# Kernel optimization log

Measured on AMD Instinct MI355X. Metric: run time of the kernel, lower is better.

## Reference

```python
import jax, jax.numpy as jnp
import numpy as np

EMB = 2048
HD = 64            # head_dim
NH = 32            # n_heads
NKV = 8            # n_kv_groups
GS = NH // NKV     # group_size = 4
WIN = 128          # sliding_window
LAYER_IDX = 0      # even -> sliding-window mask active
ROPE_BASE = 10000.0
MAX_SEQ = 4096
YARN_ORIG = 1024.0
YARN_SCALE = 4.0
YARN_BETA_FAST = 32.0
YARN_BETA_SLOW = 1.0


def _rope_tables():
    # YaRN-adjusted RoPE tables, shape [MAX_SEQ, HD]
    freqs = 1.0 / ROPE_BASE ** (np.arange(0, HD, 2, dtype=np.float32) / HD)
    wave_len = 2.0 * np.pi / freqs
    low = YARN_ORIG / YARN_BETA_FAST
    high = YARN_ORIG / YARN_BETA_SLOW
    t = np.clip((wave_len - low) / (high - low), 0.0, 1.0)
    eff = freqs * (1.0 - t) + (freqs / YARN_SCALE) * t
    conc = 0.1 * np.log(YARN_SCALE) + 1.0
    ang = (np.arange(MAX_SEQ, dtype=np.float32)[:, None] * eff[None, :]) * conc
    ang = np.concatenate([ang, ang], axis=-1).astype(np.float32)
    return jnp.sin(ang), jnp.cos(ang)


def _apply_rope(x, sin, cos):
    # x: [B, H, S, D]; sin/cos: [B, S, D] -> broadcast over heads
    sin = sin[:, None, :, :]
    cos = cos[:, None, :, :]
    x1 = x[..., : HD // 2]
    x2 = x[..., HD // 2 :]
    rotated = jnp.concatenate([-x2, x1], axis=-1)
    return x * cos + rotated * sin


def setup_inputs() -> dict:
    key = jax.random.key(0)
    ks = jax.random.split(key, 8)
    B, S = 2, 2048
    s = 0.02
    x = jax.random.normal(ks[0], (B, S, EMB), dtype=jnp.float32)
    Wq = jax.random.normal(ks[1], (NH * HD, EMB), dtype=jnp.float32) * s
    Wk = jax.random.normal(ks[2], (NKV * HD, EMB), dtype=jnp.float32) * s
    Wv = jax.random.normal(ks[3], (NKV * HD, EMB), dtype=jnp.float32) * s
    Wo = jax.random.normal(ks[4], (EMB, NH * HD), dtype=jnp.float32) * s
    bq = jnp.zeros((NH * HD,), dtype=jnp.float32)
    bk = jnp.zeros((NKV * HD,), dtype=jnp.float32)
    bv = jnp.zeros((NKV * HD,), dtype=jnp.float32)
    bo = jnp.zeros((EMB,), dtype=jnp.float32)
    sinks = jax.random.normal(ks[5], (1, NH, 1, 1), dtype=jnp.float32)
    position_ids = jnp.arange(B * S, dtype=jnp.int64 if jax.config.jax_enable_x64 else jnp.int32).reshape(B, S)
    return {"x": x, "Wq": Wq, "bq": bq, "Wk": Wk, "bk": bk, "Wv": Wv, "bv": bv,
            "Wo": Wo, "bo": bo, "sinks": sinks, "position_ids": position_ids}


def reference(x, Wq, bq, Wk, bk, Wv, bv, Wo, bo, sinks, position_ids):
    B, S, _ = x.shape
    sin_t, cos_t = _rope_tables()
    sin = sin_t[position_ids]  # [B, S, HD]
    cos = cos_t[position_ids]

    Q = (x @ Wq.T + bq).reshape(B, S, NH, HD).transpose(0, 2, 1, 3)    # [B,NH,S,D]
    K = (x @ Wk.T + bk).reshape(B, S, NKV, HD).transpose(0, 2, 1, 3)   # [B,NKV,S,D]
    V = (x @ Wv.T + bv).reshape(B, S, NKV, HD).transpose(0, 2, 1, 3)

    Q = _apply_rope(Q, sin, cos)
    K = _apply_rope(K, sin, cos)

    # GQA without materializing repeated K/V: group query heads by kv group
    Qg = Q.reshape(B, NKV, GS, S, HD)
    scores = jnp.einsum('bgqsd,bgtd->bgqst', Qg, K) / np.sqrt(HD).astype(np.float32)

    i = jnp.arange(S)[:, None]
    j = jnp.arange(S)[None, :]
    allowed = (j <= i) & (j > i - WIN)
    scores = jnp.where(allowed, scores, -jnp.inf)

    # attention-sink logit prepended before softmax, then dropped
    sink = jnp.broadcast_to(sinks.reshape(1, NKV, GS, 1, 1), (B, NKV, GS, S, 1))
    full = jnp.concatenate([sink, scores], axis=-1)
    attn = jax.nn.softmax(full, axis=-1)[..., 1:]

    ctx = jnp.einsum('bgqst,bgtd->bgqsd', attn, V)
    ctx = ctx.reshape(B, NH, S, HD).transpose(0, 2, 1, 3).reshape(B, S, NH * HD)
    out = ctx @ Wo.T + bo
    return out
```

## Files before the change

### kernel.cpp

```cpp
#include <hip/hip_runtime.h>

typedef unsigned short u16;
typedef __bf16 bf16x8 __attribute__((ext_vector_type(8)));
typedef float f32x4 __attribute__((ext_vector_type(4)));
typedef unsigned short us8 __attribute__((ext_vector_type(8)));

__device__ inline u16 f2bf(float f) {
    union { float f; unsigned u; } v; v.f = f;
    unsigned r = v.u + 0x7FFFu + ((v.u >> 16) & 1u);
    return (u16)(r >> 16);
}
__device__ inline float bf2f(u16 h) {
    union { unsigned u; float f; } v; v.u = ((unsigned)h) << 16;
    return v.f;
}
__device__ inline f32x4 mfma16(bf16x8 a, bf16x8 b, f32x4 c) {
    return __builtin_amdgcn_mfma_f32_16x16x32_bf16(a, b, c, 0, 0, 0);
}
__device__ inline void gload_lds16(const u16* g, u16* l) {
    __builtin_amdgcn_global_load_lds(
        (const __attribute__((address_space(1))) void*)g,
        (__attribute__((address_space(3))) void*)l, 16, 0, 0);
}

__global__ __launch_bounds__(256)
void pack_bf16(const float* __restrict__ src, u16* __restrict__ dst, int n)
{
    int i = (blockIdx.x * 256 + threadIdx.x) * 4;
    if (i >= n) return;
    float4 v = *(const float4*)(src + i);
    ushort4 w;
    w.x = f2bf(v.x); w.y = f2bf(v.y); w.z = f2bf(v.z); w.w = f2bf(v.w);
    *(ushort4*)(dst + i) = w;
}

__global__ __launch_bounds__(256)
void concat_bias(const float* __restrict__ bq, const float* __restrict__ bk,
                 const float* __restrict__ bv, float* __restrict__ dst)
{
    int i = blockIdx.x * 256 + threadIdx.x;
    float v;
    if (i < 2048) v = bq[i];
    else if (i < 2560) v = bk[i - 2048];
    else v = bv[i - 2560];
    dst[i] = v;
}

template<int OUT_BF16>
__global__ __launch_bounds__(256, 2)
void gemm_bb(const u16* __restrict__ A, const u16* __restrict__ B,
             const float* __restrict__ bias, void* __restrict__ Yv,
             int M, int N, int K)
{
    __shared__ u16 As[128 * 32];
    __shared__ u16 Bs[128 * 32];
    const int tid = threadIdx.x;
    const int lane = tid & 63;
    const int wv = tid >> 6;
    const int wr = wv >> 1, wc = wv & 1;
    const long m0 = (long)blockIdx.y * 128;
    const long n0 = (long)blockIdx.x * 128;
    const int cc = lane & 15, qq = lane >> 4;

    const int srow = (2 * wv) * 16 + (lane >> 2);
    const int gcol = (((lane & 3) ^ ((lane >> 3) & 3)) << 3);
    const u16* Ag0 = A + (m0 + srow) * (long)K + gcol;
    const u16* Ag1 = A + (m0 + srow + 16) * (long)K + gcol;
    const u16* Bg0 = B + (n0 + srow) * (long)K + gcol;
    const u16* Bg1 = B + (n0 + srow + 16) * (long)K + gcol;
    u16* AsW0 = &As[(2 * wv) * 512];
    u16* AsW1 = AsW0 + 512;
    u16* BsW0 = &Bs[(2 * wv) * 512];
    u16* BsW1 = BsW0 + 512;

    const int csw = (qq ^ ((cc >> 1) & 3)) << 3;

    f32x4 acc[4][4];
#pragma unroll
    for (int i = 0; i < 4; i++)
#pragma unroll
        for (int j = 0; j < 4; j++) acc[i][j] = (f32x4){0.f, 0.f, 0.f, 0.f};

    for (int k0 = 0; k0 < K; k0 += 32) {
        gload_lds16(Ag0 + k0, AsW0);
        gload_lds16(Ag1 + k0, AsW1);
        gload_lds16(Bg0 + k0, BsW0);
        gload_lds16(Bg1 + k0, BsW1);
        __syncthreads();
        bf16x8 af[4], bfr[4];
#pragma unroll
        for (int i = 0; i < 4; i++)
            af[i] = *(const bf16x8*)&As[(wr * 64 + i * 16 + cc) * 32 + csw];
#pragma unroll
        for (int j = 0; j < 4; j++)
            bfr[j] = *(const bf16x8*)&Bs[(wc * 64 + j * 16 + cc) * 32 + csw];
#pragma unroll
        for (int i = 0; i < 4; i++)
#pragma unroll
            for (int j = 0; j < 4; j++)
                acc[i][j] = mfma16(af[i], bfr[j], acc[i][j]);
        __syncthreads();
    }

#pragma unroll
    for (int i = 0; i < 4; i++) {
#pragma unroll
        for (int j = 0; j < 4; j++) {
            long row = m0 + wr * 64 + i * 16 + qq * 4;
            long col = n0 + wc * 64 + j * 16 + cc;
            float bv = bias[col];
#pragma unroll
            for (int r2 = 0; r2 < 4; r2++) {
                float v = acc[i][j][r2] + bv;
                if (OUT_BF16)
                    ((u16*)Yv)[(row + r2) * (long)N + col] = f2bf(v);
                else
                    ((float*)Yv)[(row + r2) * (long)N + col] = v;
            }
        }
    }
}

__global__ __launch_bounds__(256)
void rope_qk(const u16* __restrict__ Yt, const int* __restrict__ pid,
             u16* __restrict__ Out, int nh, int lg, int coff)
{
    int idx = blockIdx.x * 256 + threadIdx.x;
    int d = idx & 31;
    int t2 = idx >> 5;
    int hh = t2 & (nh - 1);
    int m = t2 >> lg;
    const u16* row = Yt + (size_t)m * 3072 + coff + (hh << 6);
    float x1 = bf2f(row[d]), x2 = bf2f(row[d + 32]);
    int pos = pid[m];
    float ex = (float)d * (1.0f / 32.0f);
    float freq = powf(10000.0f, -ex);
    float wl = 6.2831853071795864f / freq;
    float tt = (wl - 32.0f) * (1.0f / 992.0f);
    tt = fminf(fmaxf(tt, 0.0f), 1.0f);
    float eff = freq * (1.0f - tt) + 0.25f * freq * tt;
    float ang = ((float)pos * eff) * 1.1386294361119891f;
    float sv = sinf(ang), cv = cosf(ang);
    int b = m >> 11, s = m & 2047;
    u16* o = Out + (((size_t)(b * nh + hh)) * 2048 + s) * 64;
    o[d]      = f2bf(x1 * cv - x2 * sv);
    o[d + 32] = f2bf(x2 * cv + x1 * sv);
}

__global__ __launch_bounds__(256)
void v_transpose(const u16* __restrict__ Vt, u16* __restrict__ VbT)
{
    __shared__ u16 tile[64][66];
    int s0 = blockIdx.x * 64;
    int bkv = blockIdx.y;
    int b = bkv >> 3, kv = bkv & 7;
    int t = threadIdx.x;
#pragma unroll
    for (int it = 0; it < 16; ++it) {
        int idx = t + it * 256;
        int s = idx >> 6, d = idx & 63;
        tile[s][d] = Vt[((size_t)(b * 2048 + s0 + s)) * 3072 + 2560 + kv * 64 + d];
    }
    __syncthreads();
#pragma unroll
    for (int it = 0; it < 16; ++it) {
        int idx = t + it * 256;
        int d = idx >> 6, s = idx & 63;
        VbT[((size_t)(bkv * 64 + d)) * 2048 + s0 + s] = tile[s][d];
    }
}

__global__ __launch_bounds__(256, 2)
void attn_win(const u16* __restrict__ Qb, const u16* __restrict__ Kb,
              const u16* __restrict__ VbT, const float* __restrict__ sinks,
              u16* __restrict__ Ctx)
{
    __shared__ u16 Ks[192 * 72];
    __shared__ u16 Vs[64 * 200];
    __shared__ u16 Pb[4 * 16 * 200];
    const int S = 2048;
    const int tid = threadIdx.x;
    const int lane = tid & 63;
    const int w = tid >> 6;
    const int cc = lane & 15, qq = lane >> 4;
    const int blk = blockIdx.x;
    const int qt = blk & 31;
    const int bkv = blk >> 5;
    const int b = bkv >> 3, kv = bkv & 7;
    const int q0 = qt * 64;
    const int ks0 = q0 - 128;
    const int h = kv * 4 + w;

    const u16* KbBase = Kb + (size_t)bkv * S * 64;
#pragma unroll
    for (int it = 0; it < 6; ++it) {
        int c = tid + it * 256;
        int kk = c >> 3, c8 = (c & 7) << 3;
        int sk = ks0 + kk;
        us8 v = {0, 0, 0, 0, 0, 0, 0, 0};
        if (sk >= 0) v = *(const us8*)(KbBase + (size_t)sk * 64 + c8);
        *(us8*)&Ks[kk * 72 + c8] = v;
    }
    const u16* VtBase = VbT + (size_t)bkv * 64 * S;
#pragma unroll
    for (int it = 0; it < 6; ++it) {
        int c = tid + it * 256;
        int d = c / 24, kc = c % 24;
        int kk0 = kc << 3;
        int sk = ks0 + kk0;
        us8 v = {0, 0, 0, 0, 0, 0, 0, 0};
        if (sk >= 0) v = *(const us8*)(VtBase + (size_t)d * S + sk);
        *(us8*)&Vs[d * 200 + kk0] = v;
    }
    __syncthreads();

    const float sinkv = sinks[h];
    u16* Pw = &Pb[w * 3200];
    const u16* Qbase = Qb + ((size_t)(b * 32 + h) * S + q0) * 64;

    for (int i = 0; i < 4; ++i) {
        const u16* Qrow = Qbase + (size_t)(i * 16 + cc) * 64;
        bf16x8 aq0 = *(const bf16x8*)(Qrow + qq * 8);
        bf16x8 aq1 = *(const bf16x8*)(Qrow + 32 + qq * 8);

        f32x4 sc[12];
#pragma unroll
        for (int j = 0; j < 12; j++) sc[j] = (f32x4){0.f, 0.f, 0.f, 0.f};
#pragma unroll
        for (int j = 0; j < 12; j++) {
            bf16x8 b0 = *(const bf16x8*)&Ks[(j * 16 + cc) * 72 + qq * 8];
            bf16x8 b1 = *(const bf16x8*)&Ks[(j * 16 + cc) * 72 + 32 + qq * 8];
            sc[j] = mfma16(aq0, b0, sc[j]);
            sc[j] = mfma16(aq1, b1, sc[j]);
        }

#pragma unroll
        for (int r = 0; r < 4; ++r) {
            int qi = i * 16 + qq * 4 + r;
            float sval[12];
            float mx = -3.0e38f;
#pragma unroll
            for (int j = 0; j < 12; j++) {
                int kk = j * 16 + cc;
                float s = sc[j][r] * 0.125f;
                bool ok = (kk > qi) && (kk <= qi + 128) && (ks0 + kk >= 0);
                s = ok ? s : -3.0e38f;
                sval[j] = s;
                mx = fmaxf(mx, s);
            }
#pragma unroll
            for (int off = 1; off < 16; off <<= 1) mx = fmaxf(mx, __shfl_xor(mx, off));
            mx = fmaxf(mx, sinkv);
            float sum = 0.f;
#pragma unroll
            for (int j = 0; j < 12; j++) {
                float p = __expf(sval[j] - mx);
                sval[j] = p;
                sum += p;
            }
#pragma unroll
            for (int off = 1; off < 16; off <<= 1) sum += __shfl_xor(sum, off);
            float rden = 1.0f / (sum + __expf(sinkv - mx));
#pragma unroll
            for (int j = 0; j < 12; j++)
                Pw[(qq * 4 + r) * 200 + j * 16 + cc] = f2bf(sval[j] * rden);
        }

        f32x4 o[4];
#pragma unroll
        for (int jt = 0; jt < 4; jt++) o[jt] = (f32x4){0.f, 0.f, 0.f, 0.f};
#pragma unroll
        for (int ks = 0; ks < 6; ks++) {
            bf16x8 ap = *(const bf16x8*)&Pw[cc * 200 + ks * 32 + qq * 8];
#pragma unroll
            for (int jt = 0; jt < 4; jt++) {
                bf16x8 bv = *(const bf16x8*)&Vs[(jt * 16 + cc) * 200 + ks * 32 + qq * 8];
                o[jt] = mfma16(ap, bv, o[jt]);
            }
        }
#pragma unroll
        for (int jt = 0; jt < 4; jt++) {
#pragma unroll
            for (int r = 0; r < 4; r++) {
                size_t off = ((size_t)(b * S + q0 + i * 16 + qq * 4 + r)) * 2048
                           + h * 64 + jt * 16 + cc;
                Ctx[off] = f2bf(o[jt][r]);
            }
        }
    }
}

extern "C" void kernel_launch(void* const* d_in, const int* in_sizes, int n_in,
                              void* d_out, int out_size, void* d_ws, size_t ws_size,
                              hipStream_t stream)
{
    const float* x    = (const float*)d_in[0];
    const float* Wq   = (const float*)d_in[1];
    const float* bq   = (const float*)d_in[2];
    const float* Wk   = (const float*)d_in[3];
    const float* bk   = (const float*)d_in[4];
    const float* Wv   = (const float*)d_in[5];
    const float* bv   = (const float*)d_in[6];
    const float* Wo   = (const float*)d_in[7];
    const float* bo   = (const float*)d_in[8];
    const float* sinks = (const float*)d_in[9];
    const int*   pid  = (const int*)d_in[10];
    float* out = (float*)d_out;

    char* ws = (char*)d_ws;
    u16*   Wqkvb = (u16*)ws;
    u16*   Wob   = (u16*)(ws + 12582912);
    u16*   xQb   = (u16*)(ws + 20971520);
    u16*   QKV   = (u16*)(ws + 37748736);
    u16*   Kb    = (u16*)(ws + 62914560);
    u16*   VbT   = (u16*)(ws + 67108864);
    float* bqkv  = (float*)(ws + 71303168);

    const int M = 4096;
    pack_bf16<<<8192, 256, 0, stream>>>(x,  xQb, 8388608);
    pack_bf16<<<4096, 256, 0, stream>>>(Wq, Wqkvb, 4194304);
    pack_bf16<<<1024, 256, 0, stream>>>(Wk, Wqkvb + 4194304, 1048576);
    pack_bf16<<<1024, 256, 0, stream>>>(Wv, Wqkvb + 5242880, 1048576);
    pack_bf16<<<4096, 256, 0, stream>>>(Wo, Wob, 4194304);
    concat_bias<<<12, 256, 0, stream>>>(bq, bk, bv, bqkv);

    gemm_bb<1><<<dim3(24, 32), 256, 0, stream>>>(xQb, Wqkvb, bqkv, QKV, M, 3072, 2048);

    rope_qk<<<16384, 256, 0, stream>>>(QKV, pid, xQb, 32, 5, 0);
    rope_qk<<<4096,  256, 0, stream>>>(QKV, pid, Kb, 8, 3, 2048);
    v_transpose<<<dim3(32, 16), 256, 0, stream>>>(QKV, VbT);

    attn_win<<<512, 256, 0, stream>>>(xQb, Kb, VbT, sinks, QKV);

    gemm_bb<0><<<dim3(16, 32), 256, 0, stream>>>(QKV, Wob, bo, out, M, 2048, 2048);
}
```

Before: 297.9 us.

## Fuse RoPE into QKV GEMM epilogue and merge pack kernels into one launch

Result: slower. 640.1 us (+114.9%).

```diff
diff --git a/kernel.cpp b/kernel.cpp
--- a/kernel.cpp
+++ b/kernel.cpp
@@ -24,84 +24,146 @@
 }
 
 __global__ __launch_bounds__(256)
-void pack_bf16(const float* __restrict__ src, u16* __restrict__ dst, int n)
-{
-    int i = (blockIdx.x * 256 + threadIdx.x) * 4;
-    if (i >= n) return;
-    float4 v = *(const float4*)(src + i);
-    ushort4 w;
-    w.x = f2bf(v.x); w.y = f2bf(v.y); w.z = f2bf(v.z); w.w = f2bf(v.w);
-    *(ushort4*)(dst + i) = w;
-}
-
-__global__ __launch_bounds__(256)
-void concat_bias(const float* __restrict__ bq, const float* __restrict__ bk,
-                 const float* __restrict__ bv, float* __restrict__ dst)
-{
-    int i = blockIdx.x * 256 + threadIdx.x;
-    float v;
-    if (i < 2048) v = bq[i];
-    else if (i < 2560) v = bk[i - 2048];
-    else v = bv[i - 2560];
-    dst[i] = v;
-}
-
-template<int OUT_BF16>
+void pack_all(const float* __restrict__ x,  const float* __restrict__ Wq,
+              const float* __restrict__ Wk, const float* __restrict__ Wv,
+              const float* __restrict__ Wo, const float* __restrict__ bq,
+              const float* __restrict__ bk, const float* __restrict__ bv,
+              u16* __restrict__ xb, u16* __restrict__ Wqkvb,
+              u16* __restrict__ Wob, float* __restrict__ bqkv)
+{
+    int blk = blockIdx.x;
+    if (blk == 9216) {
+        for (int k = threadIdx.x; k < 3072; k += 256) {
+            float v;
+            if (k < 2048) v = bq[k];
+            else if (k < 2560) v = bk[k - 2048];
+            else v = bv[k - 2560];
+            bqkv[k] = v;
+        }
+        return;
+    }
+    const float* src; u16* dst; size_t off;
+    if (blk < 4096)      { src = x;  dst = xb;                 off = (size_t)blk * 2048; }
+    else if (blk < 6144) { src = Wq; dst = Wqkvb;              off = (size_t)(blk - 4096) * 2048; }
+    else if (blk < 6656) { src = Wk; dst = Wqkvb + 4194304;    off = (size_t)(blk - 6144) * 2048; }
+    else if (blk < 7168) { src = Wv; dst = Wqkvb + 5242880;    off = (size_t)(blk - 6656) * 2048; }
+    else                 { src = Wo; dst = Wob;                off = (size_t)(blk - 7168) * 2048; }
+    size_t i = off + (size_t)threadIdx.x * 8;
+    float4 v0 = *(const float4*)(src + i);
+    float4 v1 = *(const float4*)(src + i + 4);
+    us8 w;
+    w[0] = f2bf(v0.x); w[1] = f2bf(v0.y); w[2] = f2bf(v0.z); w[3] = f2bf(v0.w);
+    w[4] = f2bf(v1.x); w[5] = f2bf(v1.y); w[6] = f2bf(v1.z); w[7] = f2bf(v1.w);
+    *(us8*)(dst + i) = w;
+}
+
+#define GEMM_PROLOGUE(Aptr, Bptr, Kdim)                                        \
+    __shared__ u16 As[128 * 32];                                               \
+    __shared__ u16 Bs[128 * 32];                                               \
+    const int tid = threadIdx.x;                                               \
+    const int lane = tid & 63;                                                 \
+    const int wv = tid >> 6;                                                   \
+    const int wr = wv >> 1, wc = wv & 1;                                       \
+    const long m0 = (long)blockIdx.y * 128;                                    \
+    const long n0 = (long)blockIdx.x * 128;                                    \
+    const int cc = lane & 15, qq = lane >> 4;                                  \
+    const int srow = (2 * wv) * 16 + (lane >> 2);                              \
+    const int gcol = (((lane & 3) ^ ((lane >> 3) & 3)) << 3);                  \
+    const u16* Ag0 = Aptr + (m0 + srow) * (long)Kdim + gcol;                   \
+    const u16* Ag1 = Aptr + (m0 + srow + 16) * (long)Kdim + gcol;              \
+    const u16* Bg0 = Bptr + (n0 + srow) * (long)Kdim + gcol;                   \
+    const u16* Bg1 = Bptr + (n0 + srow + 16) * (long)Kdim + gcol;              \
+    u16* AsW0 = &As[(2 * wv) * 512];                                           \
+    u16* AsW1 = AsW0 + 512;                                                    \
+    u16* BsW0 = &Bs[(2 * wv) * 512];                                           \
+    u16* BsW1 = BsW0 + 512;                                                    \
+    const int csw = (qq ^ ((cc >> 1) & 3)) << 3;                               \
+    f32x4 acc[4][4];                                                           \
+    _Pragma("unroll") for (int i = 0; i < 4; i++)                              \
+        _Pragma("unroll") for (int j = 0; j < 4; j++)                          \
+            acc[i][j] = (f32x4){0.f, 0.f, 0.f, 0.f};                           \
+    for (int k0 = 0; k0 < Kdim; k0 += 32) {                                    \
+        gload_lds16(Ag0 + k0, AsW0);                                           \
+        gload_lds16(Ag1 + k0, AsW1);                                           \
+        gload_lds16(Bg0 + k0, BsW0);                                           \
+        gload_lds16(Bg1 + k0, BsW1);                                           \
+        __syncthreads();                                                       \
+        bf16x8 af[4], bfr[4];                                                  \
+        _Pragma("unroll") for (int i = 0; i < 4; i++)                          \
+            af[i] = *(const bf16x8*)&As[(wr * 64 + i * 16 + cc) * 32 + csw];   \
+        _Pragma("unroll") for (int j = 0; j < 4; j++)                          \
+            bfr[j] = *(const bf16x8*)&Bs[(wc * 64 + j * 16 + cc) * 32 + csw];  \
+        _Pragma("unroll") for (int i = 0; i < 4; i++)                          \
+            _Pragma("unroll") for (int j = 0; j < 4; j++)                      \
+                acc[i][j] = mfma16(af[i], bfr[j], acc[i][j]);                  \
+        __syncthreads();                                                       \
+    }
+
 __global__ __launch_bounds__(256, 2)
-void gemm_bb(const u16* __restrict__ A, const u16* __restrict__ B,
-             const float* __restrict__ bias, void* __restrict__ Yv,
-             int M, int N, int K)
-{
-    __shared__ u16 As[128 * 32];
-    __shared__ u16 Bs[128 * 32];
-    const int tid = threadIdx.x;
-    const int lane = tid & 63;
-    const int wv = tid >> 6;
-    const int wr = wv >> 1, wc = wv & 1;
-    const long m0 = (long)blockIdx.y * 128;
-    const long n0 = (long)blockIdx.x * 128;
-    const int cc = lane & 15, qq = lane >> 4;
-
-    const int srow = (2 * wv) * 16 + (lane >> 2);
-    const int gcol = (((lane & 3) ^ ((lane >> 3) & 3)) << 3);
-    const u16* Ag0 = A + (m0 + srow) * (long)K + gcol;
-    const u16* Ag1 = A + (m0 + srow + 16) * (long)K + gcol;
-    const u16* Bg0 = B + (n0 + srow) * (long)K + gcol;
-    const u16* Bg1 = B + (n0 + srow + 16) * (long)K + gcol;
-    u16* AsW0 = &As[(2 * wv) * 512];
-    u16* AsW1 = AsW0 + 512;
-    u16* BsW0 = &Bs[(2 * wv) * 512];
-    u16* BsW1 = BsW0 + 512;
-
-    const int csw = (qq ^ ((cc >> 1) & 3)) << 3;
-
-    f32x4 acc[4][4];
-#pragma unroll
-    for (int i = 0; i < 4; i++)
-#pragma unroll
-        for (int j = 0; j < 4; j++) acc[i][j] = (f32x4){0.f, 0.f, 0.f, 0.f};
-
-    for (int k0 = 0; k0 < K; k0 += 32) {
-        gload_lds16(Ag0 + k0, AsW0);
-        gload_lds16(Ag1 + k0, AsW1);
-        gload_lds16(Bg0 + k0, BsW0);
-        gload_lds16(Bg1 + k0, BsW1);
-        __syncthreads();
-        bf16x8 af[4], bfr[4];
-#pragma unroll
-        for (int i = 0; i < 4; i++)
-            af[i] = *(const bf16x8*)&As[(wr * 64 + i * 16 + cc) * 32 + csw];
-#pragma unroll
-        for (int j = 0; j < 4; j++)
-            bfr[j] = *(const bf16x8*)&Bs[(wc * 64 + j * 16 + cc) * 32 + csw];
-#pragma unroll
-        for (int i = 0; i < 4; i++)
-#pragma unroll
-            for (int j = 0; j < 4; j++)
-                acc[i][j] = mfma16(af[i], bfr[j], acc[i][j]);
-        __syncthreads();
-    }
-
+void gemm_qkv(const u16* __restrict__ A, const u16* __restrict__ B,
+              const float* __restrict__ bias, const int* __restrict__ pid,
+              u16* __restrict__ Qb, u16* __restrict__ Kb, u16* __restrict__ Vtmp)
+{
+    GEMM_PROLOGUE(A, B, 2048)
+
+    const int reg = (n0 < 2048) ? 0 : (n0 < 2560 ? 1 : 2);
+    if (reg < 2) {
+        const int hidx = (int)(n0 >> 6) + wc - (reg ? 32 : 0);
+        u16* Out = reg ? Kb : Qb;
+        const int nheads = reg ? 8 : 32;
+#pragma unroll
+        for (int j = 0; j < 2; j++) {
+            const int d = j * 16 + cc;
+            float ex = (float)d * (1.0f / 32.0f);
+            float freq = powf(10000.0f, -ex);
+            float wl = 6.2831853071795864f / freq;
+            float tt = (wl - 32.0f) * (1.0f / 992.0f);
+            tt = fminf(fmaxf(tt, 0.0f), 1.0f);
+            float eff = freq * (1.0f - tt) + 0.25f * freq * tt;
+            eff *= 1.1386294361119891f;
+            const long colL = n0 + wc * 64 + j * 16 + cc;
+            const float bL = bias[colL], bH = bias[colL + 32];
+#pragma unroll
+            for (int i = 0; i < 4; i++) {
+#pragma unroll
+                for (int r2 = 0; r2 < 4; r2++) {
+                    long m = m0 + wr * 64 + i * 16 + qq * 4 + r2;
+                    int pos = pid[m];
+                    float ang = (float)pos * eff;
+                    float sv = sinf(ang), cv = cosf(ang);
+                    float x1 = acc[i][j][r2] + bL;
+                    float x2 = acc[i][j + 2][r2] + bH;
+                    int bb = (int)(m >> 11), ss = (int)(m & 2047);
+                    size_t base = ((size_t)(bb * nheads + hidx) * 2048 + ss) * 64;
+                    Out[base + d]      = f2bf(x1 * cv - x2 * sv);
+                    Out[base + d + 32] = f2bf(x2 * cv + x1 * sv);
+                }
+            }
+        }
+    } else {
+#pragma unroll
+        for (int i = 0; i < 4; i++) {
+#pragma unroll
+            for (int j = 0; j < 4; j++) {
+                long col = n0 + wc * 64 + j * 16 + cc;
+                float bv = bias[col];
+                long vcol = col - 2560;
+#pragma unroll
+                for (int r2 = 0; r2 < 4; r2++) {
+                    long m = m0 + wr * 64 + i * 16 + qq * 4 + r2;
+                    Vtmp[m * 512 + vcol] = f2bf(acc[i][j][r2] + bv);
+                }
+            }
+        }
+    }
+}
+
+__global__ __launch_bounds__(256, 2)
+void gemm_out(const u16* __restrict__ A, const u16* __restrict__ B,
+              const float* __restrict__ bias, float* __restrict__ Y)
+{
+    GEMM_PROLOGUE(A, B, 2048)
+    const long N = 2048;
 #pragma unroll
     for (int i = 0; i < 4; i++) {
 #pragma unroll
@@ -110,41 +172,10 @@
             long col = n0 + wc * 64 + j * 16 + cc;
             float bv = bias[col];
 #pragma unroll
-            for (int r2 = 0; r2 < 4; r2++) {
-                float v = acc[i][j][r2] + bv;
-                if (OUT_BF16)
-                    ((u16*)Yv)[(row + r2) * (long)N + col] = f2bf(v);
-                else
-                    ((float*)Yv)[(row + r2) * (long)N + col] = v;
-            }
-        }
-    }
-}
-
-__global__ __launch_bounds__(256)
-void rope_qk(const u16* __restrict__ Yt, const int* __restrict__ pid,
-             u16* __restrict__ Out, int nh, int lg, int coff)
-{
-    int idx = blockIdx.x * 256 + threadIdx.x;
-    int d = idx & 31;
-    int t2 = idx >> 5;
-    int hh = t2 & (nh - 1);
-    int m = t2 >> lg;
-    const u16* row = Yt + (size_t)m * 3072 + coff + (hh << 6);
-    float x1 = bf2f(row[d]), x2 = bf2f(row[d + 32]);
-    int pos = pid[m];
-    float ex = (float)d * (1.0f / 32.0f);
-    float freq = powf(10000.0f, -ex);
-    float wl = 6.2831853071795864f / freq;
-    float tt = (wl - 32.0f) * (1.0f / 992.0f);
-    tt = fminf(fmaxf(tt, 0.0f), 1.0f);
-    float eff = freq * (1.0f - tt) + 0.25f * freq * tt;
-    float ang = ((float)pos * eff) * 1.1386294361119891f;
-    float sv = sinf(ang), cv = cosf(ang);
-    int b = m >> 11, s = m & 2047;
-    u16* o = Out + (((size_t)(b * nh + hh)) * 2048 + s) * 64;
-    o[d]      = f2bf(x1 * cv - x2 * sv);
-    o[d + 32] = f2bf(x2 * cv + x1 * sv);
+            for (int r2 = 0; r2 < 4; r2++)
+                Y[(row + r2) * N + col] = acc[i][j][r2] + bv;
+        }
+    }
 }
 
 __global__ __launch_bounds__(256)
@@ -159,7 +190,7 @@
     for (int it = 0; it < 16; ++it) {
         int idx = t + it * 256;
         int s = idx >> 6, d = idx & 63;
-        tile[s][d] = Vt[((size_t)(b * 2048 + s0 + s)) * 3072 + 2560 + kv * 64 + d];
+        tile[s][d] = Vt[((size_t)(b * 2048 + s0 + s)) * 512 + kv * 64 + d];
     }
     __syncthreads();
 #pragma unroll
@@ -186,10 +217,10 @@
     const int blk = blockIdx.x;
     const int qt = blk & 31;
     const int bkv = blk >> 5;
-    const int b = bkv >> 3, kv = bkv & 7;
+    const int b = bkv >> 3;
     const int q0 = qt * 64;
     const int ks0 = q0 - 128;
-    const int h = kv * 4 + w;
+    const int h = (bkv & 7) * 4 + w;
 
     const u16* KbBase = Kb + (size_t)bkv * S * 64;
 #pragma unroll
@@ -310,27 +341,22 @@
     char* ws = (char*)d_ws;
     u16*   Wqkvb = (u16*)ws;
     u16*   Wob   = (u16*)(ws + 12582912);
-    u16*   xQb   = (u16*)(ws + 20971520);
-    u16*   QKV   = (u16*)(ws + 37748736);
-    u16*   Kb    = (u16*)(ws + 62914560);
-    u16*   VbT   = (u16*)(ws + 67108864);
-    float* bqkv  = (float*)(ws + 71303168);
-
-    const int M = 4096;
-    pack_bf16<<<8192, 256, 0, stream>>>(x,  xQb, 8388608);
-    pack_bf16<<<4096, 256, 0, stream>>>(Wq, Wqkvb, 4194304);
-    pack_bf16<<<1024, 256, 0, stream>>>(Wk, Wqkvb + 4194304, 1048576);
-    pack_bf16<<<1024, 256, 0, stream>>>(Wv, Wqkvb + 5242880, 1048576);
-    pack_bf16<<<4096, 256, 0, stream>>>(Wo, Wob, 4194304);
-    concat_bias<<<12, 256, 0, stream>>>(bq, bk, bv, bqkv);
-
-    gemm_bb<1><<<dim3(24, 32), 256, 0, stream>>>(xQb, Wqkvb, bqkv, QKV, M, 3072, 2048);
-
-    rope_qk<<<16384, 256, 0, stream>>>(QKV, pid, xQb, 32, 5, 0);
-    rope_qk<<<4096,  256, 0, stream>>>(QKV, pid, Kb, 8, 3, 2048);
-    v_transpose<<<dim3(32, 16), 256, 0, stream>>>(QKV, VbT);
-
-    attn_win<<<512, 256, 0, stream>>>(xQb, Kb, VbT, sinks, QKV);
-
-    gemm_bb<0><<<dim3(16, 32), 256, 0, stream>>>(QKV, Wob, bo, out, M, 2048, 2048);
-}
+    u16*   xb    = (u16*)(ws + 20971520);
+    u16*   Ctx   = xb;
+    u16*   Qb    = (u16*)(ws + 37748736);
+    u16*   Kb    = (u16*)(ws + 54525952);
+    u16*   Vtmp  = (u16*)(ws + 58720256);
+    u16*   VbT   = (u16*)(ws + 62914560);
+    float* bqkv  = (float*)(ws + 67108864);
+
+    pack_all<<<9217, 256, 0, stream>>>(x, Wq, Wk, Wv, Wo, bq, bk, bv,
+                                       xb, Wqkvb, Wob, bqkv);
+
+    gemm_qkv<<<dim3(24, 32), 256, 0, stream>>>(xb, Wqkvb, bqkv, pid, Qb, Kb, Vtmp);
+
+    v_transpose<<<dim3(32, 16), 256, 0, stream>>>(Vtmp, VbT);
+
+    attn_win<<<512, 256, 0, stream>>>(Qb, Kb, VbT, sinks, Ctx);
+
+    gemm_out<<<dim3(16, 32), 256, 0, stream>>>(Ctx, Wob, bo, out);
+}
```

## Fuse RoPE into attention loads and merge pack kernels with sin/cos table

Applied to the files above, without the earlier changes.

Result: faster. 264.8 us (-11.1%).

```diff
diff --git a/kernel.cpp b/kernel.cpp
--- a/kernel.cpp
+++ b/kernel.cpp
@@ -22,28 +22,53 @@
         (const __attribute__((address_space(1))) void*)g,
         (__attribute__((address_space(3))) void*)l, 16, 0, 0);
 }
+union frag_cast { us8 u; bf16x8 b; };
 
 __global__ __launch_bounds__(256)
-void pack_bf16(const float* __restrict__ src, u16* __restrict__ dst, int n)
-{
-    int i = (blockIdx.x * 256 + threadIdx.x) * 4;
-    if (i >= n) return;
-    float4 v = *(const float4*)(src + i);
-    ushort4 w;
-    w.x = f2bf(v.x); w.y = f2bf(v.y); w.z = f2bf(v.z); w.w = f2bf(v.w);
-    *(ushort4*)(dst + i) = w;
-}
-
-__global__ __launch_bounds__(256)
-void concat_bias(const float* __restrict__ bq, const float* __restrict__ bk,
-                 const float* __restrict__ bv, float* __restrict__ dst)
-{
-    int i = blockIdx.x * 256 + threadIdx.x;
-    float v;
-    if (i < 2048) v = bq[i];
-    else if (i < 2560) v = bk[i - 2048];
-    else v = bv[i - 2560];
-    dst[i] = v;
+void pack_all(const float* __restrict__ x,  const float* __restrict__ Wq,
+              const float* __restrict__ Wk, const float* __restrict__ Wv,
+              const float* __restrict__ Wo, const float* __restrict__ bq,
+              const float* __restrict__ bk, const float* __restrict__ bv,
+              u16* __restrict__ xb, u16* __restrict__ Wqkvb,
+              u16* __restrict__ Wob, float* __restrict__ bqkv,
+              float2* __restrict__ tab)
+{
+    int blk = blockIdx.x;
+    if (blk >= 9217) {
+        int idx = (blk - 9217) * 256 + threadIdx.x;
+        int d = idx & 31, pos = idx >> 5;
+        float ex = (float)d * (1.0f / 32.0f);
+        float freq = powf(10000.0f, -ex);
+        float wl = 6.2831853071795864f / freq;
+        float tt = fminf(fmaxf((wl - 32.0f) * (1.0f / 992.0f), 0.0f), 1.0f);
+        float eff = (freq * (1.0f - tt) + 0.25f * freq * tt) * 1.1386294361119891f;
+        float ang = (float)pos * eff;
+        tab[idx] = make_float2(cosf(ang), sinf(ang));
+        return;
+    }
+    if (blk == 9216) {
+        for (int k = threadIdx.x; k < 3072; k += 256) {
+            float v;
+            if (k < 2048) v = bq[k];
+            else if (k < 2560) v = bk[k - 2048];
+            else v = bv[k - 2560];
+            bqkv[k] = v;
+        }
+        return;
+    }
+    const float* src; u16* dst; size_t off;
+    if (blk < 4096)      { src = x;  dst = xb;                 off = (size_t)blk * 2048; }
+    else if (blk < 6144) { src = Wq; dst = Wqkvb;              off = (size_t)(blk - 4096) * 2048; }
+    else if (blk < 6656) { src = Wk; dst = Wqkvb + 4194304;    off = (size_t)(blk - 6144) * 2048; }
+    else if (blk < 7168) { src = Wv; dst = Wqkvb + 5242880;    off = (size_t)(blk - 6656) * 2048; }
+    else                 { src = Wo; dst = Wob;                off = (size_t)(blk - 7168) * 2048; }
+    size_t i = off + (size_t)threadIdx.x * 8;
+    float4 v0 = *(const float4*)(src + i);
+    float4 v1 = *(const float4*)(src + i + 4);
+    us8 w;
+    w[0] = f2bf(v0.x); w[1] = f2bf(v0.y); w[2] = f2bf(v0.z); w[3] = f2bf(v0.w);
+    w[4] = f2bf(v1.x); w[5] = f2bf(v1.y); w[6] = f2bf(v1.z); w[7] = f2bf(v1.w);
+    *(us8*)(dst + i) = w;
 }
 
 template<int OUT_BF16>
@@ -122,32 +147,6 @@
 }
 
 __global__ __launch_bounds__(256)
-void rope_qk(const u16* __restrict__ Yt, const int* __restrict__ pid,
-             u16* __restrict__ Out, int nh, int lg, int coff)
-{
-    int idx = blockIdx.x * 256 + threadIdx.x;
-    int d = idx & 31;
-    int t2 = idx >> 5;
-    int hh = t2 & (nh - 1);
-    int m = t2 >> lg;
-    const u16* row = Yt + (size_t)m * 3072 + coff + (hh << 6);
-    float x1 = bf2f(row[d]), x2 = bf2f(row[d + 32]);
-    int pos = pid[m];
-    float ex = (float)d * (1.0f / 32.0f);
-    float freq = powf(10000.0f, -ex);
-    float wl = 6.2831853071795864f / freq;
-    float tt = (wl - 32.0f) * (1.0f / 992.0f);
-    tt = fminf(fmaxf(tt, 0.0f), 1.0f);
-    float eff = freq * (1.0f - tt) + 0.25f * freq * tt;
-    float ang = ((float)pos * eff) * 1.1386294361119891f;
-    float sv = sinf(ang), cv = cosf(ang);
-    int b = m >> 11, s = m & 2047;
-    u16* o = Out + (((size_t)(b * nh + hh)) * 2048 + s) * 64;
-    o[d]      = f2bf(x1 * cv - x2 * sv);
-    o[d + 32] = f2bf(x2 * cv + x1 * sv);
-}
-
-__global__ __launch_bounds__(256)
 void v_transpose(const u16* __restrict__ Vt, u16* __restrict__ VbT)
 {
     __shared__ u16 tile[64][66];
@@ -171,9 +170,9 @@
 }
 
 __global__ __launch_bounds__(256, 2)
-void attn_win(const u16* __restrict__ Qb, const u16* __restrict__ Kb,
-              const u16* __restrict__ VbT, const float* __restrict__ sinks,
-              u16* __restrict__ Ctx)
+void attn_win2(const u16* __restrict__ QKVr, const u16* __restrict__ VbT,
+               const float2* __restrict__ tab, const int* __restrict__ pid,
+               const float* __restrict__ sinks, u16* __restrict__ Ctx)
 {
     __shared__ u16 Ks[192 * 72];
     __shared__ u16 Vs[64 * 200];
@@ -191,15 +190,32 @@
     const int ks0 = q0 - 128;
     const int h = kv * 4 + w;
 
-    const u16* KbBase = Kb + (size_t)bkv * S * 64;
-#pragma unroll
-    for (int it = 0; it < 6; ++it) {
-        int c = tid + it * 256;
-        int kk = c >> 3, c8 = (c & 7) << 3;
-        int sk = ks0 + kk;
-        us8 v = {0, 0, 0, 0, 0, 0, 0, 0};
-        if (sk >= 0) v = *(const us8*)(KbBase + (size_t)sk * 64 + c8);
-        *(us8*)&Ks[kk * 72 + c8] = v;
+    {
+        const int kcol = 2048 + kv * 64;
+#pragma unroll
+        for (int it = 0; it < 3; ++it) {
+            int c = tid + it * 256;
+            int kk = c >> 2, dlo = (c & 3) << 3;
+            int sk = ks0 + kk;
+            us8 lo = {0, 0, 0, 0, 0, 0, 0, 0};
+            us8 hi = {0, 0, 0, 0, 0, 0, 0, 0};
+            if (sk >= 0) {
+                size_t rowoff = (size_t)(b * S + sk) * 3072 + kcol;
+                us8 li = *(const us8*)(QKVr + rowoff + dlo);
+                us8 hiQ = *(const us8*)(QKVr + rowoff + dlo + 32);
+                int pos = pid[b * S + sk];
+                const float2* tp = tab + pos * 32 + dlo;
+#pragma unroll
+                for (int jj = 0; jj < 8; ++jj) {
+                    float2 cs = tp[jj];
+                    float x1 = bf2f(li[jj]), x2 = bf2f(hiQ[jj]);
+                    lo[jj] = f2bf(x1 * cs.x - x2 * cs.y);
+                    hi[jj] = f2bf(x2 * cs.x + x1 * cs.y);
+                }
+            }
+            *(us8*)&Ks[kk * 72 + dlo] = lo;
+            *(us8*)&Ks[kk * 72 + dlo + 32] = hi;
+        }
     }
     const u16* VtBase = VbT + (size_t)bkv * 64 * S;
 #pragma unroll
@@ -216,12 +232,23 @@
 
     const float sinkv = sinks[h];
     u16* Pw = &Pb[w * 3200];
-    const u16* Qbase = Qb + ((size_t)(b * 32 + h) * S + q0) * 64;
 
     for (int i = 0; i < 4; ++i) {
-        const u16* Qrow = Qbase + (size_t)(i * 16 + cc) * 64;
-        bf16x8 aq0 = *(const bf16x8*)(Qrow + qq * 8);
-        bf16x8 aq1 = *(const bf16x8*)(Qrow + 32 + qq * 8);
+        int m = b * S + q0 + i * 16 + cc;
+        const u16* Qrow = QKVr + (size_t)m * 3072 + h * 64;
+        us8 qlo = *(const us8*)(Qrow + qq * 8);
+        us8 qhi = *(const us8*)(Qrow + 32 + qq * 8);
+        int pos = pid[m];
+        const float2* tp = tab + pos * 32 + qq * 8;
+        frag_cast a0, a1;
+#pragma unroll
+        for (int jj = 0; jj < 8; ++jj) {
+            float2 cs = tp[jj];
+            float x1 = bf2f(qlo[jj]), x2 = bf2f(qhi[jj]);
+            a0.u[jj] = f2bf(x1 * cs.x - x2 * cs.y);
+            a1.u[jj] = f2bf(x2 * cs.x + x1 * cs.y);
+        }
+        bf16x8 aq0 = a0.b, aq1 = a1.b;
 
         f32x4 sc[12];
 #pragma unroll
@@ -307,30 +334,26 @@
     const int*   pid  = (const int*)d_in[10];
     float* out = (float*)d_out;
 
-    char* ws = (char*)d_ws;
+    char*  ws    = (char*)d_ws;
     u16*   Wqkvb = (u16*)ws;
     u16*   Wob   = (u16*)(ws + 12582912);
-    u16*   xQb   = (u16*)(ws + 20971520);
-    u16*   QKV   = (u16*)(ws + 37748736);
-    u16*   Kb    = (u16*)(ws + 62914560);
-    u16*   VbT   = (u16*)(ws + 67108864);
-    float* bqkv  = (float*)(ws + 71303168);
-
-    const int M = 4096;
-    pack_bf16<<<8192, 256, 0, stream>>>(x,  xQb, 8388608);
-    pack_bf16<<<4096, 256, 0, stream>>>(Wq, Wqkvb, 4194304);
-    pack_bf16<<<1024, 256, 0, stream>>>(Wk, Wqkvb + 4194304, 1048576);
-    pack_bf16<<<1024, 256, 0, stream>>>(Wv, Wqkvb + 5242880, 1048576);
-    pack_bf16<<<4096, 256, 0, stream>>>(Wo, Wob, 4194304);
-    concat_bias<<<12, 256, 0, stream>>>(bq, bk, bv, bqkv);
-
-    gemm_bb<1><<<dim3(24, 32), 256, 0, stream>>>(xQb, Wqkvb, bqkv, QKV, M, 3072, 2048);
-
-    rope_qk<<<16384, 256, 0, stream>>>(QKV, pid, xQb, 32, 5, 0);
-    rope_qk<<<4096,  256, 0, stream>>>(QKV, pid, Kb, 8, 3, 2048);
-    v_transpose<<<dim3(32, 16), 256, 0, stream>>>(QKV, VbT);
-
-    attn_win<<<512, 256, 0, stream>>>(xQb, Kb, VbT, sinks, QKV);
-
-    gemm_bb<0><<<dim3(16, 32), 256, 0, stream>>>(QKV, Wob, bo, out, M, 2048, 2048);
-}
+    u16*   xb    = (u16*)(ws + 20971520);
+    u16*   Ctx   = xb;
+    u16*   QKVr  = (u16*)(ws + 37748736);
+    u16*   VbT   = (u16*)(ws + 62914560);
+    float* bqkv  = (float*)(ws + 67108864);
+    float2* tab  = (float2*)(ws + 67121152);
+
+    pack_all<<<9729, 256, 0, stream>>>(x, Wq, Wk, Wv, Wo, bq, bk, bv,
+                                       xb, Wqkvb, Wob, bqkv, tab);
+
+    gemm_bb<1><<<dim3(24, 32), 256, 0, stream>>>(xb, Wqkvb, bqkv, QKVr,
+                                                 4096, 3072, 2048);
+
+    v_transpose<<<dim3(32, 16), 256, 0, stream>>>(QKVr, VbT);
+
+    attn_win2<<<512, 256, 0, stream>>>(QKVr, VbT, tab, pid, sinks, Ctx);
+
+    gemm_bb<0><<<dim3(16, 32), 256, 0, stream>>>(Ctx, Wob, bo, out,
+                                                 4096, 2048, 2048);
+}
```
